# Performance work log

Hardware: AMD Instinct MI355X
Metric: run time of the kernel (lower is better)

The kernel has to match this reference:

```python
import jax, jax.numpy as jnp
import numpy as np

E = 512      # embed_size
H = 8        # num_heads
L = 4        # num_layers
SF = 4       # sparsity_factor
F_IN = 128   # input feature dim (nn.Linear(128, embed_size))
N_CLS = 10


def setup_inputs() -> dict:
    key = jax.random.key(0)
    ks = jax.random.split(key, 14)
    B, S = 8, 1024
    s = 0.02
    inp = {
        "x": jax.random.normal(ks[0], (B, S, F_IN), jnp.float32),
        "emb_w": jax.random.normal(ks[1], (F_IN, E), jnp.float32) * s,
        "emb_b": jnp.zeros((E,), jnp.float32),
        "Wq": jax.random.normal(ks[2], (L, E, E), jnp.float32) * s,
        "Wk": jax.random.normal(ks[3], (L, E, E), jnp.float32) * s,
        "Wv": jax.random.normal(ks[4], (L, E, E), jnp.float32) * s,
        "Wo": jax.random.normal(ks[5], (L, E, E), jnp.float32) * s,
        "bq": jnp.zeros((L, E), jnp.float32),
        "bk": jnp.zeros((L, E), jnp.float32),
        "bv": jnp.zeros((L, E), jnp.float32),
        "bo": jnp.zeros((L, E), jnp.float32),
        "fc_w": jax.random.normal(ks[6], (E, N_CLS), jnp.float32) * s,
        "fc_b": jnp.zeros((N_CLS,), jnp.float32),
    }
    return inp


def _sparse_attn(h, wq, wk, wv, wo, bq, bk, bv, bo):
    # One SparseAttention layer: per-query top-k sparsified multi-head attention.
    B, S, _ = h.shape
    d = E // H
    k = max(1, S // SF)  # keep top S/sparsity_factor keys per query
    scale = 1.0 / np.sqrt(d)

    def heads(t):  # [B,S,E] -> [B,H,S,d]
        return t.reshape(B, S, H, d).transpose(0, 2, 1, 3)

    q = heads(h @ wq + bq)
    kk = heads(h @ wk + bk)
    v = heads(h @ wv + bv)

    scores = jnp.einsum('bhqd,bhkd->bhqk', q, kk) * scale  # [B,H,S,S]
    thresh = jax.lax.top_k(scores, k)[0][..., -1:]          # k-th largest per query
    scores = jnp.where(scores >= thresh, scores, jnp.float32(-1e9))
    p = jax.nn.softmax(scores, axis=-1)
    o = jnp.einsum('bhqk,bhkd->bhqd', p, v)                 # [B,H,S,d]
    o = o.transpose(0, 2, 1, 3).reshape(B, S, E)
    return o @ wo + bo


def reference(x, emb_w, emb_b, Wq, Wk, Wv, Wo, bq, bk, bv, bo, fc_w, fc_b):
    h = x @ emb_w + emb_b  # [B,S,E]
    for l in range(L):
        h = _sparse_attn(h, Wq[l], Wk[l], Wv[l], Wo[l], bq[l], bk[l], bv[l], bo[l])
    return h.mean(axis=1) @ fc_w + fc_b  # [B,10]
```

## Files before the change

### kernel.cpp

```cpp
#include <hip/hip_runtime.h>

#define EDIM 512
#define NH 8
#define HD 64
#define SEQ 1024
#define BATCH 8
#define NLAYER 4
#define KSEL 256

typedef __attribute__((ext_vector_type(8))) short short8;
typedef __attribute__((ext_vector_type(4))) float f32x4;

__device__ __forceinline__ unsigned short bf16_rne(float f) {
    unsigned u = __float_as_uint(f);
    return (unsigned short)((u + 0x7FFFu + ((u >> 16) & 1u)) >> 16);
}
__device__ __forceinline__ float bf16_tof(unsigned short h) {
    return __uint_as_float(((unsigned)h) << 16);
}
__device__ __forceinline__ void split2(float f, unsigned short& hi, unsigned short& lo) {
    hi = bf16_rne(f);
    float r = f - bf16_tof(hi);
    lo = (unsigned short)(__float_as_uint(r) >> 16);
}
__device__ __forceinline__ void split2t(float f, unsigned short& hi, unsigned short& lo) {
    hi = (unsigned short)(__float_as_uint(f) >> 16);
    float r = f - bf16_tof(hi);
    lo = (unsigned short)(__float_as_uint(r) >> 16);
}
__device__ __forceinline__ void split8(const float* xs, short8& hi, short8& lo) {
#pragma unroll
    for (int j = 0; j < 8; ++j) {
        unsigned short h, lw;
        split2(xs[j], h, lw);
        hi[j] = (short)h; lo[j] = (short)lw;
    }
}
__device__ __forceinline__ unsigned fmap(float s) {
    int fi = __float_as_int(s);
    return (unsigned)(fi ^ ((fi >> 31) | 0x80000000));
}
__device__ __forceinline__ float funmap(unsigned u) {
    int fi = (u & 0x80000000u) ? (int)(u ^ 0x80000000u) : (int)~u;
    return __int_as_float(fi);
}

__global__ __launch_bounds__(256) void conv_a(const float* __restrict__ A,
                                              short* __restrict__ af, int K)
{
    const int t = threadIdx.x, l = t & 63;
    const int KC = K >> 5;
    const int kc = blockIdx.x * 4 + (t >> 6);
    const int mt = blockIdx.y;
    const int m = mt * 16 + (l & 15);
    const int kb = kc * 32 + ((l >> 4) << 3);
    float4 x0 = *(const float4*)(A + (size_t)m * K + kb);
    float4 x1 = *(const float4*)(A + (size_t)m * K + kb + 4);
    float xs[8] = {x0.x, x0.y, x0.z, x0.w, x1.x, x1.y, x1.z, x1.w};
    short8 hi, lo;
    split8(xs, hi, lo);
    short* dst = af + (size_t)((mt * KC + kc) * 2) * 512 + l * 8;
    *(short8*)(dst) = hi;
    *(short8*)(dst + 512) = lo;
}

__global__ __launch_bounds__(256) void conv_wall(const float* __restrict__ Wq,
                                                 const float* __restrict__ Wk,
                                                 const float* __restrict__ Wv,
                                                 const float* __restrict__ Wo,
                                                 short* __restrict__ wf)
{
    const int z = blockIdx.z;
    const int layer = z >> 2, mm = z & 3;
    const float* W = (mm == 0 ? Wq : mm == 1 ? Wk : mm == 2 ? Wv : Wo)
                     + (size_t)layer * EDIM * EDIM;
    const float sc = (mm == 0) ? 0.125f : 1.0f;
    const int t = threadIdx.x, l = t & 63;
    const int kc = blockIdx.x * 4 + (t >> 6);
    const int nt = blockIdx.y;
    const int n = nt * 16 + (l & 15);
    const int kb = kc * 32 + ((l >> 4) << 3);
    float xs[8];
#pragma unroll
    for (int j = 0; j < 8; ++j) xs[j] = W[(size_t)(kb + j) * EDIM + n] * sc;
    short8 hi, lo;
    split8(xs, hi, lo);
    short* dst = wf + (size_t)z * 524288 + (size_t)((nt * 16 + kc) * 2) * 512 + l * 8;
    *(short8*)(dst) = hi;
    *(short8*)(dst + 512) = lo;
}

__global__ __launch_bounds__(256) void conv_w1(const float* __restrict__ W,
                                               short* __restrict__ wf, int K, int N)
{
    const int t = threadIdx.x, l = t & 63;
    const int KC = K >> 5;
    const int kc = blockIdx.x * 4 + (t >> 6);
    const int nt = blockIdx.y;
    const int n = nt * 16 + (l & 15);
    const int kb = kc * 32 + ((l >> 4) << 3);
    float xs[8];
#pragma unroll
    for (int j = 0; j < 8; ++j) xs[j] = W[(size_t)(kb + j) * N + n];
    short8 hi, lo;
    split8(xs, hi, lo);
    short* dst = wf + (size_t)((nt * KC + kc) * 2) * 512 + l * 8;
    *(short8*)(dst) = hi;
    *(short8*)(dst + 512) = lo;
}

__global__ __launch_bounds__(256, 3) void gemm_af(const short* __restrict__ af_in,
                                                  const short* __restrict__ wf,
                                                  const float* __restrict__ bias,
                                                  float* __restrict__ Cout,
                                                  short* __restrict__ af_out,
                                                  int K)
{
    __shared__ float S[128 * 68];
    const int t = threadIdx.x, l = t & 63, w = t >> 6;
    const int KC = K >> 5;
    const int mt0 = blockIdx.x * 8 + (w & 1) * 4;
    const int nt0l = (w >> 1) * 2;
    f32x4 acc[4][2] = {};

#pragma unroll 2
    for (int kc = 0; kc < KC; ++kc) {
        short8 ah[4], al[4], bh[2], bl[2];
#pragma unroll
        for (int i = 0; i < 4; ++i) {
            const short* ap = af_in + (size_t)(((mt0 + i) * KC + kc) * 2) * 512 + l * 8;
            ah[i] = *(const short8*)(ap);
            al[i] = *(const short8*)(ap + 512);
        }
#pragma unroll
        for (int j = 0; j < 2; ++j) {
            const short* bp = wf + (size_t)(((blockIdx.y * 4 + nt0l + j) * KC + kc) * 2) * 512 + l * 8;
            bh[j] = *(const short8*)(bp);
            bl[j] = *(const short8*)(bp + 512);
        }
#pragma unroll
        for (int i = 0; i < 4; ++i)
#pragma unroll
            for (int j = 0; j < 2; ++j) {
                acc[i][j] = __builtin_amdgcn_mfma_f32_16x16x32_bf16(ah[i], bh[j], acc[i][j], 0, 0, 0);
                acc[i][j] = __builtin_amdgcn_mfma_f32_16x16x32_bf16(ah[i], bl[j], acc[i][j], 0, 0, 0);
                acc[i][j] = __builtin_amdgcn_mfma_f32_16x16x32_bf16(al[i], bh[j], acc[i][j], 0, 0, 0);
            }
    }
#pragma unroll
    for (int j = 0; j < 2; ++j) {
        const int cl = (nt0l + j) * 16 + (l & 15);
        const float bv = bias[blockIdx.y * 64 + cl];
#pragma unroll
        for (int i = 0; i < 4; ++i) {
            const int rl = ((w & 1) * 4 + i) * 16 + ((l >> 4) << 2);
#pragma unroll
            for (int r = 0; r < 4; ++r) {
                const float v = acc[i][j][r] + bv;
                S[(rl + r) * 68 + cl] = v;
                if (Cout)
                    Cout[(size_t)(blockIdx.x * 128 + rl + r) * EDIM + blockIdx.y * 64 + cl] = v;
            }
        }
    }
    __syncthreads();
#pragma unroll
    for (int mi = 0; mi < 2; ++mi) {
        const int mtl = w * 2 + mi;
        const int mt = blockIdx.x * 8 + mtl;
#pragma unroll
        for (int kcl = 0; kcl < 2; ++kcl) {
            const int kc = blockIdx.y * 2 + kcl;
            const float* src = &S[(mtl * 16 + (l & 15)) * 68 + kcl * 32 + ((l >> 4) << 3)];
            float4 x0 = *(const float4*)(src);
            float4 x1 = *(const float4*)(src + 4);
            float xs[8] = {x0.x, x0.y, x0.z, x0.w, x1.x, x1.y, x1.z, x1.w};
            short8 hi, lo;
            split8(xs, hi, lo);
            short* dst = af_out + (size_t)((mt * 16 + kc) * 2) * 512 + l * 8;
            *(short8*)(dst) = hi;
            *(short8*)(dst + 512) = lo;
        }
    }
}

__global__ __launch_bounds__(256, 3) void gemm_qkv(const short* __restrict__ af,
                                                   const short* __restrict__ wfl,
                                                   const float* __restrict__ bq,
                                                   const float* __restrict__ bk,
                                                   const float* __restrict__ bv,
                                                   short* __restrict__ qf,
                                                   short* __restrict__ kf,
                                                   short* __restrict__ vf)
{
    __shared__ float S[128 * 68];
    const int y = blockIdx.y;
    const int mat = y >> 3, e = y & 7;
    const short* wfm = wfl + (size_t)mat * 524288;
    const int t = threadIdx.x, l = t & 63, w = t >> 6;
    const int KC = EDIM >> 5;
    const int mt0 = blockIdx.x * 8 + (w & 1) * 4;
    const int nt0l = (w >> 1) * 2;
    f32x4 acc[4][2] = {};

#pragma unroll 2
    for (int kc = 0; kc < KC; ++kc) {
        short8 ah[4], al[4], bh[2], bl[2];
#pragma unroll
        for (int i = 0; i < 4; ++i) {
            const short* ap = af + (size_t)(((mt0 + i) * KC + kc) * 2) * 512 + l * 8;
            ah[i] = *(const short8*)(ap);
            al[i] = *(const short8*)(ap + 512);
        }
#pragma unroll
        for (int j = 0; j < 2; ++j) {
            const short* bp = wfm + (size_t)(((e * 4 + nt0l + j) * KC + kc) * 2) * 512 + l * 8;
            bh[j] = *(const short8*)(bp);
            bl[j] = *(const short8*)(bp + 512);
        }
#pragma unroll
        for (int i = 0; i < 4; ++i)
#pragma unroll
            for (int j = 0; j < 2; ++j) {
                acc[i][j] = __builtin_amdgcn_mfma_f32_16x16x32_bf16(ah[i], bh[j], acc[i][j], 0, 0, 0);
                acc[i][j] = __builtin_amdgcn_mfma_f32_16x16x32_bf16(ah[i], bl[j], acc[i][j], 0, 0, 0);
                acc[i][j] = __builtin_amdgcn_mfma_f32_16x16x32_bf16(al[i], bh[j], acc[i][j], 0, 0, 0);
            }
    }

    const int STR = (mat == 2) ? 66 : 68;
    const float* bias = mat == 0 ? bq : mat == 1 ? bk : bv;
    const float bsc = (mat == 0) ? 0.125f : 1.0f;
#pragma unroll
    for (int j = 0; j < 2; ++j) {
        const int cl = (nt0l + j) * 16 + (l & 15);
        const float bvx = bias[e * 64 + cl] * bsc;
#pragma unroll
        for (int i = 0; i < 4; ++i) {
            const int rl = ((w & 1) * 4 + i) * 16 + ((l >> 4) << 2);
#pragma unroll
            for (int r = 0; r < 4; ++r)
                S[(rl + r) * STR + cl] = acc[i][j][r] + bvx;
        }
    }
    __syncthreads();

    if (mat == 0) {
#pragma unroll
        for (int mi = 0; mi < 2; ++mi) {
            const int mtl = w * 2 + mi;
            const int mt = blockIdx.x * 8 + mtl;
#pragma unroll
            for (int kcl = 0; kcl < 2; ++kcl) {
                const int kc = e * 2 + kcl;
                const float* src = &S[(mtl * 16 + (l & 15)) * 68 + kcl * 32 + ((l >> 4) << 3)];
                float4 x0 = *(const float4*)(src);
                float4 x1 = *(const float4*)(src + 4);
                float xs[8] = {x0.x, x0.y, x0.z, x0.w, x1.x, x1.y, x1.z, x1.w};
                short8 hi, lo;
                split8(xs, hi, lo);
                short* dst = qf + (size_t)((mt * 16 + kc) * 2) * 512 + l * 8;
                *(short8*)(dst) = hi;
                *(short8*)(dst + 512) = lo;
            }
        }
        return;
    }

    const int b = blockIdx.x >> 3;
    const int bh2 = b * 8 + e;
    if (mat == 1) {
#pragma unroll
        for (int ki = 0; ki < 2; ++ki) {
            const int ktl = w * 2 + ki;
            const int kt = (blockIdx.x & 7) * 8 + ktl;
#pragma unroll
            for (int kc = 0; kc < 2; ++kc) {
                const float* src = &S[(ktl * 16 + (l & 15)) * 68 + kc * 32 + ((l >> 4) << 3)];
                float4 x0 = *(const float4*)(src);
                float4 x1 = *(const float4*)(src + 4);
                float xs[8] = {x0.x, x0.y, x0.z, x0.w, x1.x, x1.y, x1.z, x1.w};
                short8 hi, lo;
                split8(xs, hi, lo);
                short* dst = kf + (size_t)(((bh2 * 64 + kt) * 2 + kc) * 2) * 512 + l * 8;
                *(short8*)(dst) = hi;
                *(short8*)(dst + 512) = lo;
            }
        }
    } else {
        const int jc = (blockIdx.x & 7) * 4 + w;
#pragma unroll
        for (int n = 0; n < 4; ++n) {
            float xs[8];
#pragma unroll
            for (int j2 = 0; j2 < 8; ++j2)
                xs[j2] = S[(w * 32 + ((l >> 4) << 3) + j2) * 66 + n * 16 + (l & 15)];
            short8 hi, lo;
            split8(xs, hi, lo);
            short* dst = vf + (size_t)(((bh2 * 32 + jc) * 4 + n) * 2) * 512 + l * 8;
            *(short8*)(dst) = hi;
            *(short8*)(dst + 512) = lo;
        }
    }
}

#define SPART 65536
#define SSTG  69632
#define SZINV 73984

__global__ __launch_bounds__(512, 4) void attn_mfma(const short* __restrict__ QF,
                                                    const short* __restrict__ KF,
                                                    const short* __restrict__ VF,
                                                    short* __restrict__ afo)
{
    __shared__ alignas(16) unsigned char Sb[16 * 4096 + 4096 + 4352 + 64];

    const int bh = blockIdx.x, b = bh >> 3, hh = bh & 7;
    const int q0 = blockIdx.y * 16;
    const int t = threadIdx.x, l = t & 63, w = t >> 6;
    const int qmt = (b * SEQ + q0) >> 4;

    short8 aqh[2], aql[2];
#pragma unroll
    for (int kc = 0; kc < 2; ++kc) {
        const short* qp = QF + (size_t)((qmt * 16 + hh * 2 + kc) * 2) * 512 + l * 8;
        aqh[kc] = *(const short8*)(qp);
        aql[kc] = *(const short8*)(qp + 512);
    }

    {
        const short* kfb = KF + (size_t)bh * 64 * 2048;
        const int rb = (l >> 4) << 2;
        for (int i = 0; i < 8; ++i) {
            const int kt = (w << 3) + i;
            const short* kp = kfb + (size_t)kt * 2048 + l * 8;
            short8 b00 = *(const short8*)(kp);
            short8 b01 = *(const short8*)(kp + 512);
            short8 b10 = *(const short8*)(kp + 1024);
            short8 b11 = *(const short8*)(kp + 1536);
            f32x4 acc = {0.f, 0.f, 0.f, 0.f};
            acc = __builtin_amdgcn_mfma_f32_16x16x32_bf16(aqh[0], b00, acc, 0, 0, 0);
            acc = __builtin_amdgcn_mfma_f32_16x16x32_bf16(aqh[0], b01, acc, 0, 0, 0);
            acc = __builtin_amdgcn_mfma_f32_16x16x32_bf16(aql[0], b00, acc, 0, 0, 0);
            acc = __builtin_amdgcn_mfma_f32_16x16x32_bf16(aqh[1], b10, acc, 0, 0, 0);
            acc = __builtin_amdgcn_mfma_f32_16x16x32_bf16(aqh[1], b11, acc, 0, 0, 0);
            acc = __builtin_amdgcn_mfma_f32_16x16x32_bf16(aql[1], b10, acc, 0, 0, 0);
            const int col = (kt << 4) + (l & 15);
            const int cg = col >> 2, wi = col & 3;
#pragma unroll
            for (int r = 0; r < 4; ++r) {
                const int row = rb + r;
                *(float*)(Sb + row * 4096 + (((cg ^ row) << 4) | (wi << 2))) = acc[r];
            }
        }
    }
    __syncthreads();

    {
        const int r0 = w << 1, r1 = r0 + 1;

        float s0[16], s1[16];
#pragma unroll
        for (int n = 0; n < 4; ++n) {
            float4 a = *(const float4*)(Sb + r0 * 4096 + (((l + (n << 6)) ^ r0) << 4));
            float4 c = *(const float4*)(Sb + r1 * 4096 + (((l + (n << 6)) ^ r1) << 4));
            s0[n * 4 + 0] = a.x; s0[n * 4 + 1] = a.y; s0[n * 4 + 2] = a.z; s0[n * 4 + 3] = a.w;
            s1[n * 4 + 0] = c.x; s1[n * 4 + 1] = c.y; s1[n * 4 + 2] = c.z; s1[n * 4 + 3] = c.w;
        }

        float m0 = s0[0], m1 = s1[0];
#pragma unroll
        for (int i = 1; i < 16; ++i) {
            m0 = fmaxf(m0, s0[i]);
            m1 = fmaxf(m1, s1[i]);
        }
#pragma unroll
        for (int off = 32; off > 0; off >>= 1) {
            m0 = fmaxf(m0, __shfl_xor(m0, off));
            m1 = fmaxf(m1, __shfl_xor(m1, off));
        }
        const unsigned um0 = (unsigned)__builtin_amdgcn_readfirstlane((int)fmap(m0));
        const unsigned um1 = (unsigned)__builtin_amdgcn_readfirstlane((int)fmap(m1));

        unsigned T0 = 0, T1 = 0;
        bool d0 = false, d1 = false;
        for (int bit = 31; bit >= 0; --bit) {
            const unsigned msk = 1u << bit;
            if (!d0) {
                const unsigned c0 = T0 | msk;
                if (c0 <= um0) {
                    const float fc0 = funmap(c0);
                    int n0 = 0;
#pragma unroll
                    for (int i = 0; i < 16; ++i)
                        n0 += (int)__popcll(__ballot(s0[i] >= fc0));
                    if (n0 >= KSEL) { T0 = c0; d0 = (n0 == KSEL); }
                }
            }
            if (!d1) {
                const unsigned c1 = T1 | msk;
                if (c1 <= um1) {
                    const float fc1 = funmap(c1);
                    int n1 = 0;
#pragma unroll
                    for (int i = 0; i < 16; ++i)
                        n1 += (int)__popcll(__ballot(s1[i] >= fc1));
                    if (n1 >= KSEL) { T1 = c1; d1 = (n1 == KSEL); }
                }
            }
            if (d0 & d1) break;
        }
        const float fT0 = funmap(T0), fT1 = funmap(T1);

        float Z0 = 0.f, Z1 = 0.f;
#pragma unroll
        for (int n = 0; n < 4; ++n) {
            const int gg = ((l + (n << 6)) >> 1);
            short4 H, L;
            unsigned short h, lw;
            {
                float e0 = (s0[n * 4 + 0] >= fT0) ? __expf(s0[n * 4 + 0] - m0) : 0.f;
                float e1 = (s0[n * 4 + 1] >= fT0) ? __expf(s0[n * 4 + 1] - m0) : 0.f;
                float e2 = (s0[n * 4 + 2] >= fT0) ? __expf(s0[n * 4 + 2] - m0) : 0.f;
                float e3 = (s0[n * 4 + 3] >= fT0) ? __expf(s0[n * 4 + 3] - m0) : 0.f;
                Z0 += (e0 + e1) + (e2 + e3);
                split2t(e0, h, lw); H.x = (short)h; L.x = (short)lw;
                split2t(e1, h, lw); H.y = (short)h; L.y = (short)lw;
                split2t(e2, h, lw); H.z = (short)h; L.z = (short)lw;
                split2t(e3, h, lw); H.w = (short)h; L.w = (short)lw;
                unsigned char* base0 = Sb + r0 * 4096 + (((gg ^ r0) << 4) | ((l & 1) << 3));
                *(short4*)(base0) = H;
                *(short4*)(base0 + 2048) = L;
            }
            {
                float e0 = (s1[n * 4 + 0] >= fT1) ? __expf(s1[n * 4 + 0] - m1) : 0.f;
                float e1 = (s1[n * 4 + 1] >= fT1) ? __expf(s1[n * 4 + 1] - m1) : 0.f;
                float e2 = (s1[n * 4 + 2] >= fT1) ? __expf(s1[n * 4 + 2] - m1) : 0.f;
                float e3 = (s1[n * 4 + 3] >= fT1) ? __expf(s1[n * 4 + 3] - m1) : 0.f;
                Z1 += (e0 + e1) + (e2 + e3);
                split2t(e0, h, lw); H.x = (short)h; L.x = (short)lw;
                split2t(e1, h, lw); H.y = (short)h; L.y = (short)lw;
                split2t(e2, h, lw); H.z = (short)h; L.z = (short)lw;
                split2t(e3, h, lw); H.w = (short)h; L.w = (short)lw;
                unsigned char* base1 = Sb + r1 * 4096 + (((gg ^ r1) << 4) | ((l & 1) << 3));
                *(short4*)(base1) = H;
                *(short4*)(base1 + 2048) = L;
            }
        }

#pragma unroll
        for (int off = 32; off > 0; off >>= 1) {
            Z0 += __shfl_xor(Z0, off);
            Z1 += __shfl_xor(Z1, off);
        }
        if (l == 0) {
            float* zin = (float*)(Sb + SZINV);
            zin[r0] = 1.0f / Z0;
            zin[r1] = 1.0f / Z1;
        }
    }
    __syncthreads();

    f32x4 oacc = {0.f, 0.f, 0.f, 0.f};
    const int cht = w & 3;
    {
        const int hf = w >> 2;
        const short* vfb = VF + (size_t)bh * 32 * 4096 + (size_t)cht * 1024;
        const int m = l & 15, g3 = l >> 4;
        for (int jc = hf * 16; jc < hf * 16 + 16; ++jc) {
            const int gg = (jc << 2) + g3;
            const unsigned char* abase = Sb + m * 4096 + ((gg ^ m) << 4);
            short8 ph = *(const short8*)(abase);
            short8 pl = *(const short8*)(abase + 2048);
            const short* vp = vfb + (size_t)jc * 4096 + l * 8;
            short8 vh = *(const short8*)(vp);
            short8 vl = *(const short8*)(vp + 512);
            oacc = __builtin_amdgcn_mfma_f32_16x16x32_bf16(ph, vh, oacc, 0, 0, 0);
            oacc = __builtin_amdgcn_mfma_f32_16x16x32_bf16(ph, vl, oacc, 0, 0, 0);
            oacc = __builtin_amdgcn_mfma_f32_16x16x32_bf16(pl, vh, oacc, 0, 0, 0);
        }
    }
    {
        float* part = (float*)(Sb + SPART);
        const float* zin = (const float*)(Sb + SZINV);
        const int ch = l & 15, rb = (l >> 4) << 2;
        if (w >= 4) {
#pragma unroll
            for (int r = 0; r < 4; ++r)
                part[(cht * 16 + rb + r) * 16 + ch] = oacc[r];
        }
        __syncthreads();
        if (w < 4) {
            float* stage = (float*)(Sb + SSTG);
#pragma unroll
            for (int r = 0; r < 4; ++r) {
                const float v = (oacc[r] + part[(cht * 16 + rb + r) * 16 + ch]) * zin[rb + r];
                stage[(rb + r) * 68 + cht * 16 + ch] = v;
            }
        }
        __syncthreads();
    }
    if (w < 2) {
        const float* stage = (const float*)(Sb + SSTG);
        const float* src = stage + (l & 15) * 68 + w * 32 + ((l >> 4) << 3);
        float4 x0 = *(const float4*)(src);
        float4 x1 = *(const float4*)(src + 4);
        float xs[8] = {x0.x, x0.y, x0.z, x0.w, x1.x, x1.y, x1.z, x1.w};
        short8 hi, lo;
        split8(xs, hi, lo);
        const int kc = hh * 2 + w;
        short* dst = afo + (size_t)((qmt * 16 + kc) * 2) * 512 + l * 8;
        *(short8*)(dst) = hi;
        *(short8*)(dst + 512) = lo;
    }
}

__global__ __launch_bounds__(256) void mean_fc(const float* __restrict__ Hf,
                                               const float* __restrict__ fcw,
                                               const float* __restrict__ fcb,
                                               float* __restrict__ out)
{
    __shared__ float hm[EDIM];
    const int b = blockIdx.x, t = threadIdx.x;
    const float* hb = Hf + (size_t)b * SEQ * EDIM;
    float s0 = 0.f, s1 = 0.f;
    for (int s = 0; s < SEQ; ++s) {
        s0 += hb[(size_t)s * EDIM + t];
        s1 += hb[(size_t)s * EDIM + t + 256];
    }
    hm[t] = s0 * (1.0f / SEQ);
    hm[t + 256] = s1 * (1.0f / SEQ);
    __syncthreads();
    if (t < 10) {
        float acc = fcb[t];
        for (int e = 0; e < EDIM; ++e) acc += hm[e] * fcw[e * 10 + t];
        out[b * 10 + t] = acc;
    }
}

extern "C" void kernel_launch(void* const* d_in, const int* in_sizes, int n_in,
                              void* d_out, int out_size, void* d_ws, size_t ws_size,
                              hipStream_t stream)
{
    const float* x     = (const float*)d_in[0];
    const float* emb_w = (const float*)d_in[1];
    const float* emb_b = (const float*)d_in[2];
    const float* Wq    = (const float*)d_in[3];
    const float* Wk    = (const float*)d_in[4];
    const float* Wv    = (const float*)d_in[5];
    const float* Wo    = (const float*)d_in[6];
    const float* bq    = (const float*)d_in[7];
    const float* bk    = (const float*)d_in[8];
    const float* bv    = (const float*)d_in[9];
    const float* bo    = (const float*)d_in[10];
    const float* fcw   = (const float*)d_in[11];
    const float* fcb   = (const float*)d_in[12];
    float* out = (float*)d_out;
    float* ws  = (float*)d_ws;

    const size_t SZ = (size_t)BATCH * SEQ * EDIM;
    float* h   = ws;
    short* qf  = (short*)(ws + SZ);
    short* afo = (short*)(ws + 2 * SZ);
    short* afx = (short*)(ws + 3 * SZ);
    short* wfe = afx + 4 * 1024 * 1024;
    short* kf  = (short*)(ws + 4 * SZ);
    short* vf  = (short*)(ws + 5 * SZ);
    short* afh = (short*)(ws + 6 * SZ);
    short* wf  = (short*)(ws + 7 * SZ);

    const int M = BATCH * SEQ;
    const dim3 gG(M / 128, EDIM / 64);
    const dim3 gQKV(M / 128, 3 * EDIM / 64);
    const dim3 gA(BATCH * NH, SEQ / 16);

    conv_wall<<<dim3(4, 32, 16), 256, 0, stream>>>(Wq, Wk, Wv, Wo, wf);
    conv_w1<<<dim3(1, 32), 256, 0, stream>>>(emb_w, wfe, 128, EDIM);
    conv_a<<<dim3(1, M / 16), 256, 0, stream>>>(x, afx, 128);
    gemm_af<<<gG, 256, 0, stream>>>(afx, wfe, emb_b, nullptr, afh, 128);

    for (int l = 0; l < NLAYER; ++l) {
        const short* wfl = wf + (size_t)(4 * l) * 524288;
        gemm_qkv<<<gQKV, 256, 0, stream>>>(afh, wfl, bq + l * EDIM, bk + l * EDIM,
                                           bv + l * EDIM, qf, kf, vf);
        attn_mfma<<<gA, 512, 0, stream>>>(qf, kf, vf, afo);
        gemm_af<<<gG, 256, 0, stream>>>(afo, wfl + 3 * 524288, bo + l * EDIM,
                                        (l == NLAYER - 1) ? h : nullptr, afh, EDIM);
    }
    mean_fc<<<8, 256, 0, stream>>>(h, fcw, fcb, out);
}
```

Baseline: 1.059 ms.

## Process 32 queries per attention block to reuse K and V tiles

The attention kernel now handles two 16-row query tiles per block with 1024 threads. Each loaded K and V fragment then feeds MFMAs for both query tiles, which halves global K/V traffic per query and interleaves independent accumulators. The middle section (selection/softmax) is not shown, and the shared memory grows to about 128KB, which limits occupancy to one block per CU. The partial-sum reduction is reworked to combine four wave groups through reused shared memory.

```diff
diff --git a/kernel.cpp b/kernel.cpp
--- a/kernel.cpp
+++ b/kernel.cpp
@@ -304,53 +304,64 @@
     }
 }
 
-#define SPART 65536
-#define SSTG  69632
-#define SZINV 73984
-
-__global__ __launch_bounds__(512, 4) void attn_mfma(const short* __restrict__ QF,
-                                                    const short* __restrict__ KF,
-                                                    const short* __restrict__ VF,
-                                                    short* __restrict__ afo)
-{
-    __shared__ alignas(16) unsigned char Sb[16 * 4096 + 4096 + 4352 + 64];
+#define SZINV (32 * 4096)
+
+__global__ __launch_bounds__(1024, 4) void attn_mfma(const short* __restrict__ QF,
+                                                     const short* __restrict__ KF,
+                                                     const short* __restrict__ VF,
+                                                     short* __restrict__ afo)
+{
+    __shared__ alignas(16) unsigned char Sb[32 * 4096 + 128];
 
     const int bh = blockIdx.x, b = bh >> 3, hh = bh & 7;
-    const int q0 = blockIdx.y * 16;
+    const int q0 = blockIdx.y * 32;
     const int t = threadIdx.x, l = t & 63, w = t >> 6;
     const int qmt = (b * SEQ + q0) >> 4;
 
-    short8 aqh[2], aql[2];
+    short8 aqh0[2], aql0[2], aqh1[2], aql1[2];
 #pragma unroll
     for (int kc = 0; kc < 2; ++kc) {
-        const short* qp = QF + (size_t)((qmt * 16 + hh * 2 + kc) * 2) * 512 + l * 8;
-        aqh[kc] = *(const short8*)(qp);
-        aql[kc] = *(const short8*)(qp + 512);
+        const short* qp0 = QF + (size_t)((qmt * 16 + hh * 2 + kc) * 2) * 512 + l * 8;
+        const short* qp1 = QF + (size_t)(((qmt + 1) * 16 + hh * 2 + kc) * 2) * 512 + l * 8;
+        aqh0[kc] = *(const short8*)(qp0);
+        aql0[kc] = *(const short8*)(qp0 + 512);
+        aqh1[kc] = *(const short8*)(qp1);
+        aql1[kc] = *(const short8*)(qp1 + 512);
     }
 
     {
         const short* kfb = KF + (size_t)bh * 64 * 2048;
-        const int rb = (l >> 4) << 2;
-        for (int i = 0; i < 8; ++i) {
-            const int kt = (w << 3) + i;
+        const int rb4 = (l >> 4) << 2;
+#pragma unroll 2
+        for (int i = 0; i < 4; ++i) {
+            const int kt = (w << 2) + i;
             const short* kp = kfb + (size_t)kt * 2048 + l * 8;
             short8 b00 = *(const short8*)(kp);
             short8 b01 = *(const short8*)(kp + 512);
             short8 b10 = *(const short8*)(kp + 1024);
             short8 b11 = *(const short8*)(kp + 1536);
-            f32x4 acc = {0.f, 0.f, 0.f, 0.f};
-            acc = __builtin_amdgcn_mfma_f32_16x16x32_bf16(aqh[0], b00, acc, 0, 0, 0);
-            acc = __builtin_amdgcn_mfma_f32_16x16x32_bf16(aqh[0], b01, acc, 0, 0, 0);
-            acc = __builtin_amdgcn_mfma_f32_16x16x32_bf16(aql[0], b00, acc, 0, 0, 0);
-            acc = __builtin_amdgcn_mfma_f32_16x16x32_bf16(aqh[1], b10, acc, 0, 0, 0);
-            acc = __builtin_amdgcn_mfma_f32_16x16x32_bf16(aqh[1], b11, acc, 0, 0, 0);
-            acc = __builtin_amdgcn_mfma_f32_16x16x32_bf16(aql[1], b10, acc, 0, 0, 0);
+            f32x4 a0 = {0.f, 0.f, 0.f, 0.f};
+            f32x4 a1 = {0.f, 0.f, 0.f, 0.f};
+            a0 = __builtin_amdgcn_mfma_f32_16x16x32_bf16(aqh0[0], b00, a0, 0, 0, 0);
+            a1 = __builtin_amdgcn_mfma_f32_16x16x32_bf16(aqh1[0], b00, a1, 0, 0, 0);
+            a0 = __builtin_amdgcn_mfma_f32_16x16x32_bf16(aqh0[0], b01, a0, 0, 0, 0);
+            a1 = __builtin_amdgcn_mfma_f32_16x16x32_bf16(aqh1[0], b01, a1, 0, 0, 0);
+            a0 = __builtin_amdgcn_mfma_f32_16x16x32_bf16(aql0[0], b00, a0, 0, 0, 0);
+            a1 = __builtin_amdgcn_mfma_f32_16x16x32_bf16(aql1[0], b00, a1, 0, 0, 0);
+            a0 = __builtin_amdgcn_mfma_f32_16x16x32_bf16(aqh0[1], b10, a0, 0, 0, 0);
+            a1 = __builtin_amdgcn_mfma_f32_16x16x32_bf16(aqh1[1], b10, a1, 0, 0, 0);
+            a0 = __builtin_amdgcn_mfma_f32_16x16x32_bf16(aqh0[1], b11, a0, 0, 0, 0);
+            a1 = __builtin_amdgcn_mfma_f32_16x16x32_bf16(aqh1[1], b11, a1, 0, 0, 0);
+            a0 = __builtin_amdgcn_mfma_f32_16x16x32_bf16(aql0[1], b10, a0, 0, 0, 0);
+            a1 = __builtin_amdgcn_mfma_f32_16x16x32_bf16(aql1[1], b10, a1, 0, 0, 0);
             const int col = (kt << 4) + (l & 15);
             const int cg = col >> 2, wi = col & 3;
 #pragma unroll
             for (int r = 0; r < 4; ++r) {
-                const int row = rb + r;
-                *(float*)(Sb + row * 4096 + (((cg ^ row) << 4) | (wi << 2))) = acc[r];
+                const int row0 = rb4 + r;
+                const int row1 = 16 + rb4 + r;
+                *(float*)(Sb + row0 * 4096 + (((cg ^ row0) << 4) | (wi << 2))) = a0[r];
+                *(float*)(Sb + row1 * 4096 + (((cg ^ row1) << 4) | (wi << 2))) = a1[r];
             }
         }
     }
@@ -461,57 +472,76 @@
     }
     __syncthreads();
 
-    f32x4 oacc = {0.f, 0.f, 0.f, 0.f};
-    const int cht = w & 3;
+    f32x4 oc0 = {0.f, 0.f, 0.f, 0.f};
+    f32x4 oc1 = {0.f, 0.f, 0.f, 0.f};
+    const int cht = w & 3, jcq = w >> 2;
     {
-        const int hf = w >> 2;
         const short* vfb = VF + (size_t)bh * 32 * 4096 + (size_t)cht * 1024;
         const int m = l & 15, g3 = l >> 4;
-        for (int jc = hf * 16; jc < hf * 16 + 16; ++jc) {
-            const int gg = (jc << 2) + g3;
-            const unsigned char* abase = Sb + m * 4096 + ((gg ^ m) << 4);
-            short8 ph = *(const short8*)(abase);
-            short8 pl = *(const short8*)(abase + 2048);
+#pragma unroll 2
+        for (int i = 0; i < 8; ++i) {
+            const int jc = (jcq << 3) + i;
             const short* vp = vfb + (size_t)jc * 4096 + l * 8;
             short8 vh = *(const short8*)(vp);
             short8 vl = *(const short8*)(vp + 512);
-            oacc = __builtin_amdgcn_mfma_f32_16x16x32_bf16(ph, vh, oacc, 0, 0, 0);
-            oacc = __builtin_amdgcn_mfma_f32_16x16x32_bf16(ph, vl, oacc, 0, 0, 0);
-            oacc = __builtin_amdgcn_mfma_f32_16x16x32_bf16(pl, vh, oacc, 0, 0, 0);
-        }
-    }
+            const int gg = (jc << 2) + g3;
+            const int row0 = m, row1 = 16 + m;
+            const unsigned char* ab0 = Sb + row0 * 4096 + ((gg ^ row0) << 4);
+            const unsigned char* ab1 = Sb + row1 * 4096 + ((gg ^ row1) << 4);
+            short8 p0h = *(const short8*)(ab0);
+            short8 p0l = *(const short8*)(ab0 + 2048);
+            short8 p1h = *(const short8*)(ab1);
+            short8 p1l = *(const short8*)(ab1 + 2048);
+            oc0 = __builtin_amdgcn_mfma_f32_16x16x32_bf16(p0h, vh, oc0, 0, 0, 0);
+            oc1 = __builtin_amdgcn_mfma_f32_16x16x32_bf16(p1h, vh, oc1, 0, 0, 0);
+            oc0 = __builtin_amdgcn_mfma_f32_16x16x32_bf16(p0h, vl, oc0, 0, 0, 0);
+            oc1 = __builtin_amdgcn_mfma_f32_16x16x32_bf16(p1h, vl, oc1, 0, 0, 0);
+            oc0 = __builtin_amdgcn_mfma_f32_16x16x32_bf16(p0l, vh, oc0, 0, 0, 0);
+            oc1 = __builtin_amdgcn_mfma_f32_16x16x32_bf16(p1l, vh, oc1, 0, 0, 0);
+        }
+    }
+    __syncthreads();
+
     {
-        float* part = (float*)(Sb + SPART);
+        float* part = (float*)(Sb);
+        const int ch = l & 15, rb4 = (l >> 4) << 2;
+        if (jcq != 0) {
+#pragma unroll
+            for (int r = 0; r < 4; ++r) {
+                part[(((cht * 2 + 0) * 3 + (jcq - 1)) << 8) + (rb4 + r) * 16 + ch] = oc0[r];
+                part[(((cht * 2 + 1) * 3 + (jcq - 1)) << 8) + (rb4 + r) * 16 + ch] = oc1[r];
+            }
+        }
+        __syncthreads();
+        float* stage = (float*)(Sb + 24576);
         const float* zin = (const float*)(Sb + SZINV);
-        const int ch = l & 15, rb = (l >> 4) << 2;
-        if (w >= 4) {
-#pragma unroll
-            for (int r = 0; r < 4; ++r)
-                part[(cht * 16 + rb + r) * 16 + ch] = oacc[r];
+        if (jcq == 0) {
+#pragma unroll
+            for (int r = 0; r < 4; ++r) {
+                float v0 = oc0[r], v1 = oc1[r];
+#pragma unroll
+                for (int p = 0; p < 3; ++p) {
+                    v0 += part[(((cht * 2 + 0) * 3 + p) << 8) + (rb4 + r) * 16 + ch];
+                    v1 += part[(((cht * 2 + 1) * 3 + p) << 8) + (rb4 + r) * 16 + ch];
+                }
+                stage[(rb4 + r) * 68 + cht * 16 + ch] = v0 * zin[rb4 + r];
+                stage[(16 + rb4 + r) * 68 + cht * 16 + ch] = v1 * zin[16 + rb4 + r];
+            }
         }
         __syncthreads();
         if (w < 4) {
-            float* stage = (float*)(Sb + SSTG);
-#pragma unroll
-            for (int r = 0; r < 4; ++r) {
-                const float v = (oacc[r] + part[(cht * 16 + rb + r) * 16 + ch]) * zin[rb + r];
-                stage[(rb + r) * 68 + cht * 16 + ch] = v;
-            }
-        }
-        __syncthreads();
-    }
-    if (w < 2) {
-        const float* stage = (const float*)(Sb + SSTG);
-        const float* src = stage + (l & 15) * 68 + w * 32 + ((l >> 4) << 3);
-        float4 x0 = *(const float4*)(src);
-        float4 x1 = *(const float4*)(src + 4);
-        float xs[8] = {x0.x, x0.y, x0.z, x0.w, x1.x, x1.y, x1.z, x1.w};
-        short8 hi, lo;
-        split8(xs, hi, lo);
-        const int kc = hh * 2 + w;
-        short* dst = afo + (size_t)((qmt * 16 + kc) * 2) * 512 + l * 8;
-        *(short8*)(dst) = hi;
-        *(short8*)(dst + 512) = lo;
+            const int mtl = w >> 1, kcl = w & 1;
+            const float* src = stage + (mtl * 16 + (l & 15)) * 68 + kcl * 32 + ((l >> 4) << 3);
+            float4 x0 = *(const float4*)(src);
+            float4 x1 = *(const float4*)(src + 4);
+            float xs[8] = {x0.x, x0.y, x0.z, x0.w, x1.x, x1.y, x1.z, x1.w};
+            short8 hi, lo;
+            split8(xs, hi, lo);
+            const int kc = hh * 2 + kcl;
+            short* dst = afo + (size_t)(((qmt + mtl) * 16 + kc) * 2) * 512 + l * 8;
+            *(short8*)(dst) = hi;
+            *(short8*)(dst + 512) = lo;
+        }
     }
 }
 
@@ -572,7 +602,7 @@
     const int M = BATCH * SEQ;
     const dim3 gG(M / 128, EDIM / 64);
     const dim3 gQKV(M / 128, 3 * EDIM / 64);
-    const dim3 gA(BATCH * NH, SEQ / 16);
+    const dim3 gA(BATCH * NH, SEQ / 32);
 
     conv_wall<<<dim3(4, 32, 16), 256, 0, stream>>>(Wq, Wk, Wv, Wo, wf);
     conv_w1<<<dim3(1, 32), 256, 0, stream>>>(emb_w, wfe, 128, EDIM);
@@ -583,7 +613,7 @@
         const short* wfl = wf + (size_t)(4 * l) * 524288;
         gemm_qkv<<<gQKV, 256, 0, stream>>>(afh, wfl, bq + l * EDIM, bk + l * EDIM,
                                            bv + l * EDIM, qf, kf, vf);
-        attn_mfma<<<gA, 512, 0, stream>>>(qf, kf, vf, afo);
+        attn_mfma<<<gA, 1024, 0, stream>>>(qf, kf, vf, afo);
         gemm_af<<<gG, 256, 0, stream>>>(afo, wfl + 3 * 524288, bo + l * EDIM,
                                         (l == NLAYER - 1) ? h : nullptr, afh, EDIM);
     }
```

Result: slower. 1.173 ms (+10.7%).
